# Kernel optimization log

Measured on AMD Instinct MI355X. Metric: run time of the kernel, lower is better.

The kernel has to match this reference:

```python
import jax, jax.numpy as jnp
import numpy as np

BETA = 0.25


def setup_inputs() -> dict:
    key = jax.random.key(0)
    k1, k2, k3, k4 = jax.random.split(key, 4)
    e_dim, n_e = 512, 8192
    z = jax.random.normal(k1, (16, e_dim, 32, 32), dtype=jnp.float32)
    # nn.init.normal_(embedding.weight, std=e_dim**-0.5)
    emb_weight = jax.random.normal(k2, (n_e, e_dim), dtype=jnp.float32) * (e_dim ** -0.5)
    # torch Linear default init ~ U(-1/sqrt(in), 1/sqrt(in))
    lim = 1.0 / np.sqrt(e_dim)
    proj_w = jax.random.uniform(k3, (e_dim, e_dim), minval=-lim, maxval=lim, dtype=jnp.float32)
    proj_b = jax.random.uniform(k4, (e_dim,), minval=-lim, maxval=lim, dtype=jnp.float32)
    return {"z": z, "emb_weight": emb_weight, "proj_w": proj_w, "proj_b": proj_b}


def reference(z, emb_weight, proj_w, proj_b):
    # z: [B, C, H, W] -> [B, H, W, C]
    zc = jnp.transpose(z, (0, 2, 3, 1))
    B, H, W, C = zc.shape
    z_flat = zc.reshape(-1, C)                               # [N, C]
    # projected codebook: Linear(e_dim, e_dim) -> x @ W^T + b
    qc = emb_weight @ proj_w.T + proj_b                      # [n_e, C]
    # squared distances: ||z||^2 + ||qc||^2 - 2 z.qc
    d = (jnp.sum(z_flat ** 2, axis=1, keepdims=True)
         + jnp.sum(qc ** 2, axis=1)
         - 2.0 * jnp.einsum('nd,kd->nk', z_flat, qc))        # [N, n_e]
    idx = jnp.argmin(d, axis=1)                              # [N]
    z_q = qc[idx].reshape(zc.shape)                          # [B, H, W, C]
    # legacy=False commit loss
    commit_loss = (BETA * jnp.mean((jax.lax.stop_gradient(z_q) - zc) ** 2)
                   + jnp.mean((z_q - jax.lax.stop_gradient(zc)) ** 2))
    # straight-through
    z_q = zc + jax.lax.stop_gradient(z_q - zc)
    z_q = jnp.transpose(z_q, (0, 3, 1, 2))                   # [B, C, H, W]
    min_encoding_indices = idx.reshape(B, H, W)              # sane_index_shape=True
    return z_q, commit_loss, min_encoding_indices
```

## Files before the change

### kernel.cpp

```cpp
#include <hip/hip_runtime.h>

typedef unsigned int uint;
typedef unsigned short ushort;
typedef __attribute__((ext_vector_type(8))) short short8;
typedef __attribute__((ext_vector_type(4))) float f32x4;

#define B_   16
#define C_   512
#define HW_  1024
#define N_   16384
#define K_   8192
#define EPS_ 0.25f

#define QC_OFF    0u
#define QC_SZ     (K_ * C_)
#define QN_OFF    (QC_OFF + QC_SZ)
#define QN_SZ     K_
#define ZN_OFF    (QN_OFF + QN_SZ)
#define ZN_SZ     N_
#define ZF_OFF    (ZN_OFF + ZN_SZ)
#define ZF_SZ     (N_ * C_)
#define ZH_OFF    (ZF_OFF + ZF_SZ)
#define ZH_SZ     (N_ * C_ / 2)
#define QH_OFF    (ZH_OFF + ZH_SZ)
#define QH_SZ     (K_ * C_ / 2)
#define WT_OFF    (QH_OFF + QH_SZ)
#define WT_SZ     (64 * N_ * 4)
#define CK_OFF    (WT_OFF + WT_SZ)
#define CK_SZ     (N_ * 16)
#define CC_OFF    (CK_OFF + CK_SZ)
#define CC_SZ     N_
#define IDXF_OFF  (CC_OFF + CC_SZ)
#define IDXF_SZ   N_
#define LOSS_OFF  (IDXF_OFF + IDXF_SZ)

#define OUT_ZQ    0
#define OUT_LOSS  8388608
#define OUT_IDX   8388609

__device__ __forceinline__ ushort f2bf(float f) {
    uint x = __float_as_uint(f);
    uint r = x + 0x7fffu + ((x >> 16) & 1u);
    return (ushort)(r >> 16);
}

__global__ __launch_bounds__(256) void transpose_z(const float* __restrict__ z,
                                                   float* __restrict__ zf,
                                                   ushort* __restrict__ zh) {
    __shared__ float ld[64][65];
    const int t = threadIdx.x;
    const int mt = blockIdx.x, ct = blockIdx.y, b = blockIdx.z;
    {
        const int cl = t >> 4, m4 = (t & 15) * 4;
#pragma unroll
        for (int cc = 0; cc < 4; ++cc) {
            const int c = ct * 64 + cc * 16 + cl;
            float4 v = *(const float4*)&z[((size_t)(b * 512 + c)) * 1024 + mt * 64 + m4];
            ld[cc * 16 + cl][m4 + 0] = v.x; ld[cc * 16 + cl][m4 + 1] = v.y;
            ld[cc * 16 + cl][m4 + 2] = v.z; ld[cc * 16 + cl][m4 + 3] = v.w;
        }
    }
    __syncthreads();
    {
        const int nl = t >> 4, c4 = (t & 15) * 4;
#pragma unroll
        for (int nn = 0; nn < 4; ++nn) {
            const int n_local = nn * 16 + nl;
            const size_t n = (size_t)b * 1024 + mt * 64 + n_local;
            float4 w;
            w.x = ld[c4 + 0][n_local]; w.y = ld[c4 + 1][n_local];
            w.z = ld[c4 + 2][n_local]; w.w = ld[c4 + 3][n_local];
            *(float4*)&zf[n * 512 + ct * 64 + c4] = w;
            ushort4 h; h.x = f2bf(w.x); h.y = f2bf(w.y); h.z = f2bf(w.z); h.w = f2bf(w.w);
            *(ushort4*)&zh[n * 512 + ct * 64 + c4] = h;
        }
    }
}

__global__ __launch_bounds__(256) void qc_gemm(const float* __restrict__ emb,
                                               const float* __restrict__ W,
                                               const float* __restrict__ bias,
                                               float* __restrict__ qc,
                                               ushort* __restrict__ qh) {
    __shared__ float As[16][132];
    __shared__ float Bs[16][68];
    const int t    = threadIdx.x;
    const int k0   = blockIdx.x * 128;
    const int c0   = blockIdx.y * 64;
    const int ty   = t >> 4, tx = t & 15;
    const int rowA = t >> 1;
    const int dqA  = (t & 1) * 8;
    const int rowB = t >> 2;
    const int dqB  = (t & 3) * 4;

    const float* pa = emb + (size_t)(k0 + rowA) * 512 + dqA;
    const float* pb = W   + (size_t)(c0 + rowB) * 512 + dqB;
    float4 ra0 = *(const float4*)&pa[0];
    float4 ra1 = *(const float4*)&pa[4];
    float4 rb  = *(const float4*)&pb[0];

    float acc[2][4][4] = {};
    for (int d0 = 0; d0 < 512; d0 += 16) {
        __syncthreads();
        As[dqA + 0][rowA] = ra0.x; As[dqA + 1][rowA] = ra0.y;
        As[dqA + 2][rowA] = ra0.z; As[dqA + 3][rowA] = ra0.w;
        As[dqA + 4][rowA] = ra1.x; As[dqA + 5][rowA] = ra1.y;
        As[dqA + 6][rowA] = ra1.z; As[dqA + 7][rowA] = ra1.w;
        Bs[dqB + 0][rowB] = rb.x;  Bs[dqB + 1][rowB] = rb.y;
        Bs[dqB + 2][rowB] = rb.z;  Bs[dqB + 3][rowB] = rb.w;
        if (d0 + 16 < 512) {
            ra0 = *(const float4*)&pa[d0 + 16];
            ra1 = *(const float4*)&pa[d0 + 20];
            rb  = *(const float4*)&pb[d0 + 16];
        }
        __syncthreads();
#pragma unroll
        for (int dd = 0; dd < 16; ++dd) {
            float4 a0 = *(const float4*)&As[dd][ty * 4];
            float4 a1 = *(const float4*)&As[dd][64 + ty * 4];
            float4 b0 = *(const float4*)&Bs[dd][tx * 4];
            float aa[2][4] = {{a0.x, a0.y, a0.z, a0.w}, {a1.x, a1.y, a1.z, a1.w}};
            float bb[4] = {b0.x, b0.y, b0.z, b0.w};
#pragma unroll
            for (int ih = 0; ih < 2; ++ih)
#pragma unroll
                for (int i = 0; i < 4; ++i)
#pragma unroll
                    for (int j = 0; j < 4; ++j)
                        acc[ih][i][j] += aa[ih][i] * bb[j];
        }
    }
#pragma unroll
    for (int ih = 0; ih < 2; ++ih)
#pragma unroll
        for (int i = 0; i < 4; ++i) {
            const size_t kr = (size_t)(k0 + ih * 64 + ty * 4 + i) * 512;
            const int cb = c0 + tx * 4;
            float4 v;
            v.x = acc[ih][i][0] + bias[cb + 0];
            v.y = acc[ih][i][1] + bias[cb + 1];
            v.z = acc[ih][i][2] + bias[cb + 2];
            v.w = acc[ih][i][3] + bias[cb + 3];
            *(float4*)&qc[kr + cb] = v;
            ushort4 h; h.x = f2bf(v.x); h.y = f2bf(v.y); h.z = f2bf(v.z); h.w = f2bf(v.w);
            *(ushort4*)&qh[kr + cb] = h;
        }
}

__global__ __launch_bounds__(256) void znorm_pairwise(const float* __restrict__ z,
                                                      float* __restrict__ zn) {
#pragma clang fp contract(off)
    const int n = blockIdx.x * 256 + threadIdx.x;
    const int b = n >> 10, m = n & 1023;
    const float* base = z + (size_t)b * C_ * HW_ + m;
    float s128[4];
#pragma unroll
    for (int blk = 0; blk < 4; ++blk) {
        float r[8];
#pragma unroll
        for (int j = 0; j < 8; ++j) {
            float v = base[(size_t)(blk * 128 + j) * HW_];
            r[j] = v * v;
        }
#pragma unroll 1
        for (int i = 8; i < 128; i += 8) {
#pragma unroll
            for (int j = 0; j < 8; ++j) {
                float v = base[(size_t)(blk * 128 + i + j) * HW_];
                float sq = v * v;
                r[j] = r[j] + sq;
            }
        }
        s128[blk] = ((r[0] + r[1]) + (r[2] + r[3])) + ((r[4] + r[5]) + (r[6] + r[7]));
    }
    zn[n] = (s128[0] + s128[1]) + (s128[2] + s128[3]);
}

__global__ __launch_bounds__(256) void qnorm_grouped(const float* __restrict__ qc,
                                                     float* __restrict__ qn) {
#pragma clang fp contract(off)
    const int t   = threadIdx.x;
    const int grp = t >> 3;
    const int j   = t & 7;
    const int k   = blockIdx.x * 32 + grp;
    const float* row = qc + (size_t)k * C_;
    float s[4];
#pragma unroll
    for (int blk = 0; blk < 4; ++blk) {
        float v0 = row[blk * 128 + j];
        float r  = v0 * v0;
#pragma unroll 1
        for (int i = 1; i < 16; ++i) {
            float v  = row[blk * 128 + i * 8 + j];
            float sq = v * v;
            r = r + sq;
        }
        float t1 = r  + __shfl_xor(r, 1, 64);
        float t2 = t1 + __shfl_xor(t1, 2, 64);
        float t3 = t2 + __shfl_xor(t2, 4, 64);
        s[blk] = t3;
    }
    if (j == 0) qn[k] = (s[0] + s[1]) + (s[2] + s[3]);
}

#define PH_BAR()  __builtin_amdgcn_s_barrier()
#define PH_LGKM() asm volatile("s_waitcnt lgkmcnt(0)" ::: "memory")
#define PH_VM4()  asm volatile("s_waitcnt vmcnt(4)" ::: "memory")

__device__ __forceinline__ short8 ld8(const short* p, int off) {
    return *(const short8*)(p + off);
}

__global__ __launch_bounds__(512, 2) void phaseA(const ushort* __restrict__ qh,
                                                 const ushort* __restrict__ zh,
                                                 const float* __restrict__ qn,
                                                 float* __restrict__ wtop) {
    __shared__ short lq[32768];
    __shared__ short lz[32768];
    const int t    = threadIdx.x;
    const int lane = t & 63;
    const int wv   = t >> 6;
    const int wk   = wv >> 2;
    const int wn   = wv & 3;
    const int n0   = blockIdx.x * 256;
    const int k0   = blockIdx.y * 256;

    const int l15 = lane & 15;
    const int hi8 = (lane >> 4) << 3;
    const int xr  = (l15 & 7) << 3;
    const short* pA0 = lq + wk * 8192 + l15 * 64 + ((hi8) ^ xr);
    const short* pA1 = lq + wk * 8192 + l15 * 64 + ((32 + hi8) ^ xr);
    const short* pB0 = lz + (wn >> 1) * 8192 + (wn & 1) * 4096 + l15 * 64 + ((hi8) ^ xr);
    const short* pB1 = lz + (wn >> 1) * 8192 + (wn & 1) * 4096 + l15 * 64 + ((32 + hi8) ^ xr);

    const int ch0 = t,        row0 = ch0 >> 3;
    const int ch1 = t + 512,  row1 = ch1 >> 3;
    const int ce0 = ((ch0 ^ row0) & 7) << 3;
    const int ce1 = ((ch1 ^ row1) & 7) << 3;
    const ushort* qsrc0 = qh + (size_t)(k0 + row0) * 512 + ce0;
    const ushort* qsrc1 = qh + (size_t)(k0 + row1) * 512 + ce1;
    const ushort* zsrc0 = zh + (size_t)(n0 + row0) * 512 + ce0;
    const ushort* zsrc1 = zh + (size_t)(n0 + row1) * 512 + ce1;
    short* qdst0 = lq + ch0 * 8;
    short* qdst1 = lq + ch1 * 8;
    short* zdst0 = lz + ch0 * 8;
    short* zdst1 = lz + ch1 * 8;

    auto stage_half = [&](int b, int h, int chunk) {
        const int co = chunk * 64;
        if (h < 2) {
            __builtin_amdgcn_global_load_lds(
                (const __attribute__((address_space(1))) uint*)(qsrc0 + h * 65536 + co),
                (__attribute__((address_space(3))) uint*)(qdst0 + (b * 2 + h) * 8192), 16, 0, 0);
            __builtin_amdgcn_global_load_lds(
                (const __attribute__((address_space(1))) uint*)(qsrc1 + h * 65536 + co),
                (__attribute__((address_space(3))) uint*)(qdst1 + (b * 2 + h) * 8192), 16, 0, 0);
        } else {
            __builtin_amdgcn_global_load_lds(
                (const __attribute__((address_space(1))) uint*)(zsrc0 + (h - 2) * 65536 + co),
                (__attribute__((address_space(3))) uint*)(zdst0 + (b * 2 + (h - 2)) * 8192), 16, 0, 0);
            __builtin_amdgcn_global_load_lds(
                (const __attribute__((address_space(1))) uint*)(zsrc1 + (h - 2) * 65536 + co),
                (__attribute__((address_space(3))) uint*)(zdst1 + (b * 2 + (h - 2)) * 8192), 16, 0, 0);
        }
    };

    f32x4 acc[8][4];
#pragma unroll
    for (int i = 0; i < 8; ++i)
#pragma unroll
        for (int j = 0; j < 4; ++j) acc[i][j] = (f32x4){0.f, 0.f, 0.f, 0.f};

    stage_half(0, 0, 0); stage_half(0, 1, 0); stage_half(0, 2, 0); stage_half(0, 3, 0);
    stage_half(1, 0, 1); stage_half(1, 1, 1);
    PH_VM4();
    PH_BAR();

    short8 a0[2][4], a1[2][4], b0[2][2], b1[2][2];

#pragma unroll 1
    for (int I = 0; I < 4; ++I) {
        const int t1 = 2 * I + 1;
        const int t2 = (2 * I + 2) & 7;
        const int t3 = (2 * I + 3) & 7;

#pragma unroll
        for (int i = 0; i < 4; ++i) { a0[0][i] = ld8(pA0, i * 1024); a0[1][i] = ld8(pA1, i * 1024); }
#pragma unroll
        for (int jj = 0; jj < 2; ++jj) { b0[0][jj] = ld8(pB0, jj * 1024); b0[1][jj] = ld8(pB1, jj * 1024); }
        stage_half(1, 2, t1);
        PH_BAR(); PH_LGKM();
        __builtin_amdgcn_s_setprio(1);
#pragma unroll
        for (int kk = 0; kk < 2; ++kk)
#pragma unroll
            for (int i = 0; i < 4; ++i)
#pragma unroll
                for (int jj = 0; jj < 2; ++jj)
                    acc[i][jj] = __builtin_amdgcn_mfma_f32_16x16x32_bf16(a0[kk][i], b0[kk][jj], acc[i][jj], 0, 0, 0);
        __builtin_amdgcn_s_setprio(0);
        PH_BAR();
#pragma unroll
        for (int i = 0; i < 4; ++i) { a1[0][i] = ld8(pA0, 4096 + i * 1024); a1[1][i] = ld8(pA1, 4096 + i * 1024); }
        stage_half(1, 3, t1);
        PH_BAR(); PH_LGKM();
        __builtin_amdgcn_s_setprio(1);
#pragma unroll
        for (int kk = 0; kk < 2; ++kk)
#pragma unroll
            for (int i = 0; i < 4; ++i)
#pragma unroll
                for (int jj = 0; jj < 2; ++jj)
                    acc[4 + i][jj] = __builtin_amdgcn_mfma_f32_16x16x32_bf16(a1[kk][i], b0[kk][jj], acc[4 + i][jj], 0, 0, 0);
        __builtin_amdgcn_s_setprio(0);
        PH_BAR();
#pragma unroll
        for (int jj = 0; jj < 2; ++jj) { b1[0][jj] = ld8(pB0, 2048 + jj * 1024); b1[1][jj] = ld8(pB1, 2048 + jj * 1024); }
        stage_half(0, 0, t2);
        PH_BAR(); PH_LGKM();
        __builtin_amdgcn_s_setprio(1);
#pragma unroll
        for (int kk = 0; kk < 2; ++kk)
#pragma unroll
            for (int i = 0; i < 4; ++i)
#pragma unroll
                for (int jj = 0; jj < 2; ++jj)
                    acc[i][2 + jj] = __builtin_amdgcn_mfma_f32_16x16x32_bf16(a0[kk][i], b1[kk][jj], acc[i][2 + jj], 0, 0, 0);
        __builtin_amdgcn_s_setprio(0);
        PH_BAR();
        stage_half(0, 1, t2);
        PH_BAR(); PH_LGKM();
        __builtin_amdgcn_s_setprio(1);
#pragma unroll
        for (int kk = 0; kk < 2; ++kk)
#pragma unroll
            for (int i = 0; i < 4; ++i)
#pragma unroll
                for (int jj = 0; jj < 2; ++jj)
                    acc[4 + i][2 + jj] = __builtin_amdgcn_mfma_f32_16x16x32_bf16(a1[kk][i], b1[kk][jj], acc[4 + i][2 + jj], 0, 0, 0);
        __builtin_amdgcn_s_setprio(0);
        PH_VM4();
        PH_BAR();

#pragma unroll
        for (int i = 0; i < 4; ++i) { a0[0][i] = ld8(pA0, 16384 + i * 1024); a0[1][i] = ld8(pA1, 16384 + i * 1024); }
#pragma unroll
        for (int jj = 0; jj < 2; ++jj) { b0[0][jj] = ld8(pB0, 16384 + jj * 1024); b0[1][jj] = ld8(pB1, 16384 + jj * 1024); }
        stage_half(0, 2, t2);
        PH_BAR(); PH_LGKM();
        __builtin_amdgcn_s_setprio(1);
#pragma unroll
        for (int kk = 0; kk < 2; ++kk)
#pragma unroll
            for (int i = 0; i < 4; ++i)
#pragma unroll
                for (int jj = 0; jj < 2; ++jj)
                    acc[i][jj] = __builtin_amdgcn_mfma_f32_16x16x32_bf16(a0[kk][i], b0[kk][jj], acc[i][jj], 0, 0, 0);
        __builtin_amdgcn_s_setprio(0);
        PH_BAR();
#pragma unroll
        for (int i = 0; i < 4; ++i) { a1[0][i] = ld8(pA0, 16384 + 4096 + i * 1024); a1[1][i] = ld8(pA1, 16384 + 4096 + i * 1024); }
        stage_half(0, 3, t2);
        PH_BAR(); PH_LGKM();
        __builtin_amdgcn_s_setprio(1);
#pragma unroll
        for (int kk = 0; kk < 2; ++kk)
#pragma unroll
            for (int i = 0; i < 4; ++i)
#pragma unroll
                for (int jj = 0; jj < 2; ++jj)
                    acc[4 + i][jj] = __builtin_amdgcn_mfma_f32_16x16x32_bf16(a1[kk][i], b0[kk][jj], acc[4 + i][jj], 0, 0, 0);
        __builtin_amdgcn_s_setprio(0);
        PH_BAR();
#pragma unroll
        for (int jj = 0; jj < 2; ++jj) { b1[0][jj] = ld8(pB0, 16384 + 2048 + jj * 1024); b1[1][jj] = ld8(pB1, 16384 + 2048 + jj * 1024); }
        stage_half(1, 0, t3);
        PH_BAR(); PH_LGKM();
        __builtin_amdgcn_s_setprio(1);
#pragma unroll
        for (int kk = 0; kk < 2; ++kk)
#pragma unroll
            for (int i = 0; i < 4; ++i)
#pragma unroll
                for (int jj = 0; jj < 2; ++jj)
                    acc[i][2 + jj] = __builtin_amdgcn_mfma_f32_16x16x32_bf16(a0[kk][i], b1[kk][jj], acc[i][2 + jj], 0, 0, 0);
        __builtin_amdgcn_s_setprio(0);
        PH_BAR();
        stage_half(1, 1, t3);
        PH_BAR(); PH_LGKM();
        __builtin_amdgcn_s_setprio(1);
#pragma unroll
        for (int kk = 0; kk < 2; ++kk)
#pragma unroll
            for (int i = 0; i < 4; ++i)
#pragma unroll
                for (int jj = 0; jj < 2; ++jj)
                    acc[4 + i][2 + jj] = __builtin_amdgcn_mfma_f32_16x16x32_bf16(a1[kk][i], b1[kk][jj], acc[4 + i][2 + jj], 0, 0, 0);
        __builtin_amdgcn_s_setprio(0);
        PH_VM4();
        PH_BAR();
    }

    const int q4 = (lane >> 4) * 4;
    float v1[4], v2[4];
    int   k1[4], k2[4];
#pragma unroll
    for (int in = 0; in < 4; ++in) { v1[in] = 1e30f; v2[in] = 1e30f; k1[in] = 0; k2[in] = 0; }

#pragma unroll
    for (int ik = 0; ik < 8; ++ik) {
        float qv[4];
#pragma unroll
        for (int r = 0; r < 4; ++r)
            qv[r] = qn[k0 + wk * 128 + ik * 16 + q4 + r];
#pragma unroll
        for (int in = 0; in < 4; ++in) {
#pragma unroll
            for (int r = 0; r < 4; ++r) {
                const float val = qv[r] - 2.0f * acc[ik][in][r];
                const int   kg  = k0 + wk * 128 + ik * 16 + q4 + r;
                if (val < v1[in]) { v2[in] = v1[in]; k2[in] = k1[in]; v1[in] = val; k1[in] = kg; }
                else if (val < v2[in]) { v2[in] = val; k2[in] = kg; }
            }
        }
    }
#pragma unroll
    for (int m = 16; m <= 32; m <<= 1) {
#pragma unroll
        for (int in = 0; in < 4; ++in) {
            const float ov1 = __shfl_xor(v1[in], m, 64);
            const int   ok1 = __shfl_xor(k1[in], m, 64);
            const float ov2 = __shfl_xor(v2[in], m, 64);
            const int   ok2 = __shfl_xor(k2[in], m, 64);
            float nv1, nv2; int nk1, nk2;
            if (ov1 < v1[in]) {
                nv1 = ov1; nk1 = ok1;
                if (v1[in] < ov2) { nv2 = v1[in]; nk2 = k1[in]; } else { nv2 = ov2; nk2 = ok2; }
            } else {
                nv1 = v1[in]; nk1 = k1[in];
                if (ov1 < v2[in]) { nv2 = ov1; nk2 = ok1; } else { nv2 = v2[in]; nk2 = k2[in]; }
            }
            v1[in] = nv1; k1[in] = nk1; v2[in] = nv2; k2[in] = nk2;
        }
    }
    if ((lane >> 4) == 0) {
        const int w = blockIdx.y * 2 + wk;
#pragma unroll
        for (int in = 0; in < 4; ++in) {
            const int n = n0 + wn * 64 + in * 16 + (lane & 15);
            float4 o; o.x = v1[in]; o.y = __int_as_float(k1[in]);
            o.z = v2[in]; o.w = __int_as_float(k2[in]);
            *(float4*)&wtop[((size_t)w * N_ + n) * 4] = o;
        }
    }
}

__global__ __launch_bounds__(256) void phaseB(const float* __restrict__ wtop,
                                              int* __restrict__ cand_k,
                                              int* __restrict__ cand_cnt,
                                              float* __restrict__ loss_acc) {
    const int n = blockIdx.x * 256 + threadIdx.x;
    if (n == 0) loss_acc[0] = 0.f;
    float rmin = 1e30f;
    for (int w = 0; w < 64; ++w)
        rmin = fminf(rmin, wtop[((size_t)w * N_ + n) * 4]);
    const float thr = rmin + EPS_;
    int cnt = 0;
    for (int w = 0; w < 64; ++w) {
        float4 e = *(const float4*)&wtop[((size_t)w * N_ + n) * 4];
        if (e.x <= thr && cnt < 16) cand_k[n * 16 + cnt++] = __float_as_int(e.y);
        if (e.z <= thr && cnt < 16) cand_k[n * 16 + cnt++] = __float_as_int(e.w);
    }
    cand_cnt[n] = cnt;
}

__global__ __launch_bounds__(256) void phaseC(const float* __restrict__ zf,
                                              const float* __restrict__ qc,
                                              const float* __restrict__ zn,
                                              const float* __restrict__ qn,
                                              const int* __restrict__ cand_k,
                                              const int* __restrict__ cand_cnt,
                                              int* __restrict__ idxf,
                                              float* __restrict__ out_idx) {
    __shared__ float zr[4][512];
    __shared__ float ql[4][2][512];
    const int wv   = threadIdx.x >> 6;
    const int lane = threadIdx.x & 63;
    const int r    = blockIdx.x * 4 + wv;
    const int cnt  = cand_cnt[r];

    if (cnt == 1) {
        if (lane == 0) { const int k = cand_k[r * 16]; idxf[r] = k; out_idx[r] = (float)k; }
        return;
    }

    *(float4*)&zr[wv][lane * 8]     = *(const float4*)&zf[(size_t)r * 512 + lane * 8];
    *(float4*)&zr[wv][lane * 8 + 4] = *(const float4*)&zf[(size_t)r * 512 + lane * 8 + 4];

    const int g  = lane >> 5;
    const int cl = (lane & 31) * 16;
    const int steps = (cnt + 1) >> 1;
    const float znr = zn[r];

    auto cand_of = [&](int s) {
        const int ci = 2 * s + g;
        return cand_k[r * 16 + (ci < cnt ? ci : 0)];
    };

    int k_cur = cand_of(0);
    const float* q0 = qc + (size_t)k_cur * 512 + cl;
    float4 p0 = *(const float4*)&q0[0];
    float4 p1 = *(const float4*)&q0[4];
    float4 p2 = *(const float4*)&q0[8];
    float4 p3 = *(const float4*)&q0[12];

    float bd = 1e30f;
    int   bi = 0x7fffffff;

    for (int s = 0; s < steps; ++s) {
        *(float4*)&ql[wv][g][cl + 0]  = p0;
        *(float4*)&ql[wv][g][cl + 4]  = p1;
        *(float4*)&ql[wv][g][cl + 8]  = p2;
        *(float4*)&ql[wv][g][cl + 12] = p3;

        int k_next = 0;
        if (s + 1 < steps) {
            k_next = cand_of(s + 1);
            const float* qn_ = qc + (size_t)k_next * 512 + cl;
            p0 = *(const float4*)&qn_[0];
            p1 = *(const float4*)&qn_[4];
            p2 = *(const float4*)&qn_[8];
            p3 = *(const float4*)&qn_[12];
        }

        float acc = 0.f;
#pragma unroll 16
        for (int c = 0; c < 512; c += 4) {
            float4 zv = *(const float4*)&zr[wv][c];
            float4 qv = *(const float4*)&ql[wv][g][c];
            acc = fmaf(zv.x, qv.x, acc);
            acc = fmaf(zv.y, qv.y, acc);
            acc = fmaf(zv.z, qv.z, acc);
            acc = fmaf(zv.w, qv.w, acc);
        }
        const float T = znr + qn[k_cur];
        const float d = T - 2.0f * acc;
        const bool valid = (2 * s + g) < cnt;
        if (valid && (d < bd || (d == bd && k_cur < bi))) { bd = d; bi = k_cur; }
        k_cur = k_next;
    }

    const float od = __shfl_xor(bd, 32, 64);
    const int   oi = __shfl_xor(bi, 32, 64);
    if (od < bd || (od == bd && oi < bi)) { bd = od; bi = oi; }

    if (lane == 0) { idxf[r] = bi; out_idx[r] = (float)bi; }
}

__global__ __launch_bounds__(256) void gather_out(const float* __restrict__ z,
                                                  const float* __restrict__ qc,
                                                  const int* __restrict__ idxf,
                                                  float* __restrict__ zq_out,
                                                  float* __restrict__ loss_acc) {
    __shared__ int   idxs[64];
    __shared__ float zqs[64][65];
    __shared__ float wsum[4];
    const int t  = threadIdx.x;
    const int mc = blockIdx.x;
    const int cc = blockIdx.y;
    const int bz = blockIdx.z;

    if (t < 64) idxs[t] = idxf[bz * 1024 + mc * 64 + t];
    __syncthreads();
    {
        const int row  = t >> 2;
        const int coff = (t & 3) * 16;
        const float* src = qc + (size_t)idxs[row] * 512 + cc * 64 + coff;
#pragma unroll
        for (int v = 0; v < 4; ++v) {
            float4 q = *(const float4*)&src[v * 4];
            zqs[row][coff + v * 4 + 0] = q.x;
            zqs[row][coff + v * 4 + 1] = q.y;
            zqs[row][coff + v * 4 + 2] = q.z;
            zqs[row][coff + v * 4 + 3] = q.w;
        }
    }
    __syncthreads();

    float ls = 0.f;
    {
        const int c_local = t >> 2;
        const int mg      = (t & 3) * 16;
        const size_t gbase = ((size_t)(bz * 512 + cc * 64 + c_local)) * 1024 + mc * 64 + mg;
#pragma unroll
        for (int v = 0; v < 4; ++v) {
            const int m = mg + v * 4;
            float4 w;
            w.x = zqs[m + 0][c_local];
            w.y = zqs[m + 1][c_local];
            w.z = zqs[m + 2][c_local];
            w.w = zqs[m + 3][c_local];
            float4 zv = *(const float4*)&z[gbase + v * 4];
            float dx = w.x - zv.x, dy = w.y - zv.y, dz = w.z - zv.z, dw = w.w - zv.w;
            ls += dx * dx + dy * dy + dz * dz + dw * dw;
            *(float4*)&zq_out[gbase + v * 4] = w;
        }
    }
#pragma unroll
    for (int m = 32; m; m >>= 1) ls += __shfl_xor(ls, m, 64);
    const int lane = t & 63, wvv = t >> 6;
    if (lane == 0) wsum[wvv] = ls;
    __syncthreads();
    if (t == 0) atomicAdd(loss_acc, wsum[0] + wsum[1] + wsum[2] + wsum[3]);
}

__global__ void finalize(const float* __restrict__ loss_acc,
                         float* __restrict__ out_loss) {
    out_loss[0] = 1.25f * loss_acc[0] / 8388608.0f;
}

extern "C" void kernel_launch(void* const* d_in, const int* in_sizes, int n_in,
                              void* d_out, int out_size, void* d_ws, size_t ws_size,
                              hipStream_t stream) {
    const float* z    = (const float*)d_in[0];
    const float* emb  = (const float*)d_in[1];
    const float* W    = (const float*)d_in[2];
    const float* bias = (const float*)d_in[3];
    float* ws = (float*)d_ws;

    float*  qc       = ws + QC_OFF;
    float*  qn       = ws + QN_OFF;
    float*  zn       = ws + ZN_OFF;
    float*  zf       = ws + ZF_OFF;
    ushort* zh       = (ushort*)(ws + ZH_OFF);
    ushort* qh       = (ushort*)(ws + QH_OFF);
    float*  wtop     = ws + WT_OFF;
    int*    cand_k   = (int*)(ws + CK_OFF);
    int*    cand_cnt = (int*)(ws + CC_OFF);
    int*    idxf     = (int*)(ws + IDXF_OFF);
    float*  loss_acc = ws + LOSS_OFF;
    float*  out      = (float*)d_out;

    transpose_z<<<dim3(16, 8, 16), 256, 0, stream>>>(z, zf, zh);
    qc_gemm<<<dim3(K_ / 128, C_ / 64), 256, 0, stream>>>(emb, W, bias, qc, qh);
    qnorm_grouped<<<K_ / 32, 256, 0, stream>>>(qc, qn);
    znorm_pairwise<<<N_ / 256, 256, 0, stream>>>(z, zn);
    phaseA<<<dim3(N_ / 256, K_ / 256), 512, 0, stream>>>(qh, zh, qn, wtop);
    phaseB<<<N_ / 256, 256, 0, stream>>>(wtop, cand_k, cand_cnt, loss_acc);
    phaseC<<<N_ / 4, 256, 0, stream>>>(zf, qc, zn, qn, cand_k, cand_cnt, idxf, out + OUT_IDX);
    gather_out<<<dim3(16, 8, B_), 256, 0, stream>>>(z, qc, idxf, out + OUT_ZQ, loss_acc);
    finalize<<<1, 1, 0, stream>>>(loss_acc, out + OUT_LOSS);
}
```

Measured before the change: 419.7 us.

## Fuse candidate selection into refinement kernel and restructure phaseA MFMA schedule

Merges phaseB (per-row threshold and candidate list) into phaseC by having each wavefront read its row's 64 per-tile top-2 entries, reduce the minimum with shuffles, and compact candidates into LDS via ballot/popcount. This removes a kernel launch and the global cand_k/cand_cnt round trip. wtop is re-laid out row-major so each row's entries are contiguous. phaseA's inner loop is restructured from four barrier-separated MFMA sub-phases to two larger ones, staging two halves per phase with a partial lgkmcnt wait. The candidate cap of 16 is removed (up to 128 now), which could change work for rows with many near-ties.

```diff
diff --git a/kernel.cpp b/kernel.cpp
--- a/kernel.cpp
+++ b/kernel.cpp
@@ -2,6 +2,7 @@
 
 typedef unsigned int uint;
 typedef unsigned short ushort;
+typedef unsigned long long ulong64;
 typedef __attribute__((ext_vector_type(8))) short short8;
 typedef __attribute__((ext_vector_type(4))) float f32x4;
 
@@ -26,11 +27,7 @@
 #define QH_SZ     (K_ * C_ / 2)
 #define WT_OFF    (QH_OFF + QH_SZ)
 #define WT_SZ     (64 * N_ * 4)
-#define CK_OFF    (WT_OFF + WT_SZ)
-#define CK_SZ     (N_ * 16)
-#define CC_OFF    (CK_OFF + CK_SZ)
-#define CC_SZ     N_
-#define IDXF_OFF  (CC_OFF + CC_SZ)
+#define IDXF_OFF  (WT_OFF + WT_SZ)
 #define IDXF_SZ   N_
 #define LOSS_OFF  (IDXF_OFF + IDXF_SZ)
 
@@ -203,9 +200,10 @@
     if (j == 0) qn[k] = (s[0] + s[1]) + (s[2] + s[3]);
 }
 
-#define PH_BAR()  __builtin_amdgcn_s_barrier()
-#define PH_LGKM() asm volatile("s_waitcnt lgkmcnt(0)" ::: "memory")
-#define PH_VM4()  asm volatile("s_waitcnt vmcnt(4)" ::: "memory")
+#define PH_BAR()   __builtin_amdgcn_s_barrier()
+#define PH_LGKM()  asm volatile("s_waitcnt lgkmcnt(0)" ::: "memory")
+#define PH_LGKM8() asm volatile("s_waitcnt lgkmcnt(8)" ::: "memory")
+#define PH_VM4()   asm volatile("s_waitcnt vmcnt(4)" ::: "memory")
 
 __device__ __forceinline__ short8 ld8(const short* p, int off) {
     return *(const short8*)(p + off);
@@ -280,15 +278,18 @@
 
 #pragma unroll 1
     for (int I = 0; I < 4; ++I) {
-        const int t1 = 2 * I + 1;
-        const int t2 = (2 * I + 2) & 7;
-        const int t3 = (2 * I + 3) & 7;
-
-#pragma unroll
-        for (int i = 0; i < 4; ++i) { a0[0][i] = ld8(pA0, i * 1024); a0[1][i] = ld8(pA1, i * 1024); }
+        const int tE = 2 * I;
+        const int tO = 2 * I + 1;
+
+#pragma unroll
+        for (int i = 0; i < 4; ++i) {
+            a0[0][i] = ld8(pA0, i * 1024);        a0[1][i] = ld8(pA1, i * 1024);
+            a1[0][i] = ld8(pA0, 4096 + i * 1024); a1[1][i] = ld8(pA1, 4096 + i * 1024);
+        }
 #pragma unroll
         for (int jj = 0; jj < 2; ++jj) { b0[0][jj] = ld8(pB0, jj * 1024); b0[1][jj] = ld8(pB1, jj * 1024); }
-        stage_half(1, 2, t1);
+        stage_half(1, 2, (tO) & 7); stage_half(1, 3, (tO) & 7);
+        PH_LGKM8();
         PH_BAR(); PH_LGKM();
         __builtin_amdgcn_s_setprio(1);
 #pragma unroll
@@ -296,13 +297,15 @@
 #pragma unroll
             for (int i = 0; i < 4; ++i)
 #pragma unroll
-                for (int jj = 0; jj < 2; ++jj)
-                    acc[i][jj] = __builtin_amdgcn_mfma_f32_16x16x32_bf16(a0[kk][i], b0[kk][jj], acc[i][jj], 0, 0, 0);
+                for (int jj = 0; jj < 2; ++jj) {
+                    acc[i][jj]     = __builtin_amdgcn_mfma_f32_16x16x32_bf16(a0[kk][i], b0[kk][jj], acc[i][jj], 0, 0, 0);
+                    acc[4 + i][jj] = __builtin_amdgcn_mfma_f32_16x16x32_bf16(a1[kk][i], b0[kk][jj], acc[4 + i][jj], 0, 0, 0);
+                }
         __builtin_amdgcn_s_setprio(0);
         PH_BAR();
 #pragma unroll
-        for (int i = 0; i < 4; ++i) { a1[0][i] = ld8(pA0, 4096 + i * 1024); a1[1][i] = ld8(pA1, 4096 + i * 1024); }
-        stage_half(1, 3, t1);
+        for (int jj = 0; jj < 2; ++jj) { b1[0][jj] = ld8(pB0, 2048 + jj * 1024); b1[1][jj] = ld8(pB1, 2048 + jj * 1024); }
+        stage_half(0, 0, (tE + 2) & 7); stage_half(0, 1, (tE + 2) & 7);
         PH_BAR(); PH_LGKM();
         __builtin_amdgcn_s_setprio(1);
 #pragma unroll
@@ -310,43 +313,23 @@
 #pragma unroll
             for (int i = 0; i < 4; ++i)
 #pragma unroll
-                for (int jj = 0; jj < 2; ++jj)
-                    acc[4 + i][jj] = __builtin_amdgcn_mfma_f32_16x16x32_bf16(a1[kk][i], b0[kk][jj], acc[4 + i][jj], 0, 0, 0);
-        __builtin_amdgcn_s_setprio(0);
-        PH_BAR();
-#pragma unroll
-        for (int jj = 0; jj < 2; ++jj) { b1[0][jj] = ld8(pB0, 2048 + jj * 1024); b1[1][jj] = ld8(pB1, 2048 + jj * 1024); }
-        stage_half(0, 0, t2);
-        PH_BAR(); PH_LGKM();
-        __builtin_amdgcn_s_setprio(1);
-#pragma unroll
-        for (int kk = 0; kk < 2; ++kk)
-#pragma unroll
-            for (int i = 0; i < 4; ++i)
-#pragma unroll
-                for (int jj = 0; jj < 2; ++jj)
-                    acc[i][2 + jj] = __builtin_amdgcn_mfma_f32_16x16x32_bf16(a0[kk][i], b1[kk][jj], acc[i][2 + jj], 0, 0, 0);
-        __builtin_amdgcn_s_setprio(0);
-        PH_BAR();
-        stage_half(0, 1, t2);
-        PH_BAR(); PH_LGKM();
-        __builtin_amdgcn_s_setprio(1);
-#pragma unroll
-        for (int kk = 0; kk < 2; ++kk)
-#pragma unroll
-            for (int i = 0; i < 4; ++i)
-#pragma unroll
-                for (int jj = 0; jj < 2; ++jj)
+                for (int jj = 0; jj < 2; ++jj) {
+                    acc[i][2 + jj]     = __builtin_amdgcn_mfma_f32_16x16x32_bf16(a0[kk][i], b1[kk][jj], acc[i][2 + jj], 0, 0, 0);
                     acc[4 + i][2 + jj] = __builtin_amdgcn_mfma_f32_16x16x32_bf16(a1[kk][i], b1[kk][jj], acc[4 + i][2 + jj], 0, 0, 0);
+                }
         __builtin_amdgcn_s_setprio(0);
         PH_VM4();
         PH_BAR();
 
 #pragma unroll
-        for (int i = 0; i < 4; ++i) { a0[0][i] = ld8(pA0, 16384 + i * 1024); a0[1][i] = ld8(pA1, 16384 + i * 1024); }
+        for (int i = 0; i < 4; ++i) {
+            a0[0][i] = ld8(pA0, 16384 + i * 1024);        a0[1][i] = ld8(pA1, 16384 + i * 1024);
+            a1[0][i] = ld8(pA0, 16384 + 4096 + i * 1024); a1[1][i] = ld8(pA1, 16384 + 4096 + i * 1024);
+        }
 #pragma unroll
         for (int jj = 0; jj < 2; ++jj) { b0[0][jj] = ld8(pB0, 16384 + jj * 1024); b0[1][jj] = ld8(pB1, 16384 + jj * 1024); }
-        stage_half(0, 2, t2);
+        stage_half(0, 2, (tO + 1) & 7); stage_half(0, 3, (tO + 1) & 7);
+        PH_LGKM8();
         PH_BAR(); PH_LGKM();
         __builtin_amdgcn_s_setprio(1);
 #pragma unroll
@@ -354,13 +337,15 @@
 #pragma unroll
             for (int i = 0; i < 4; ++i)
 #pragma unroll
-                for (int jj = 0; jj < 2; ++jj)
-                    acc[i][jj] = __builtin_amdgcn_mfma_f32_16x16x32_bf16(a0[kk][i], b0[kk][jj], acc[i][jj], 0, 0, 0);
+                for (int jj = 0; jj < 2; ++jj) {
+                    acc[i][jj]     = __builtin_amdgcn_mfma_f32_16x16x32_bf16(a0[kk][i], b0[kk][jj], acc[i][jj], 0, 0, 0);
+                    acc[4 + i][jj] = __builtin_amdgcn_mfma_f32_16x16x32_bf16(a1[kk][i], b0[kk][jj], acc[4 + i][jj], 0, 0, 0);
+                }
         __builtin_amdgcn_s_setprio(0);
         PH_BAR();
 #pragma unroll
-        for (int i = 0; i < 4; ++i) { a1[0][i] = ld8(pA0, 16384 + 4096 + i * 1024); a1[1][i] = ld8(pA1, 16384 + 4096 + i * 1024); }
-        stage_half(0, 3, t2);
+        for (int jj = 0; jj < 2; ++jj) { b1[0][jj] = ld8(pB0, 16384 + 2048 + jj * 1024); b1[1][jj] = ld8(pB1, 16384 + 2048 + jj * 1024); }
+        stage_half(1, 0, (tO + 2) & 7); stage_half(1, 1, (tO + 2) & 7);
         PH_BAR(); PH_LGKM();
         __builtin_amdgcn_s_setprio(1);
 #pragma unroll
@@ -368,34 +353,10 @@
 #pragma unroll
             for (int i = 0; i < 4; ++i)
 #pragma unroll
-                for (int jj = 0; jj < 2; ++jj)
-                    acc[4 + i][jj] = __builtin_amdgcn_mfma_f32_16x16x32_bf16(a1[kk][i], b0[kk][jj], acc[4 + i][jj], 0, 0, 0);
-        __builtin_amdgcn_s_setprio(0);
-        PH_BAR();
-#pragma unroll
-        for (int jj = 0; jj < 2; ++jj) { b1[0][jj] = ld8(pB0, 16384 + 2048 + jj * 1024); b1[1][jj] = ld8(pB1, 16384 + 2048 + jj * 1024); }
-        stage_half(1, 0, t3);
-        PH_BAR(); PH_LGKM();
-        __builtin_amdgcn_s_setprio(1);
-#pragma unroll
-        for (int kk = 0; kk < 2; ++kk)
-#pragma unroll
-            for (int i = 0; i < 4; ++i)
-#pragma unroll
-                for (int jj = 0; jj < 2; ++jj)
-                    acc[i][2 + jj] = __builtin_amdgcn_mfma_f32_16x16x32_bf16(a0[kk][i], b1[kk][jj], acc[i][2 + jj], 0, 0, 0);
-        __builtin_amdgcn_s_setprio(0);
-        PH_BAR();
-        stage_half(1, 1, t3);
-        PH_BAR(); PH_LGKM();
-        __builtin_amdgcn_s_setprio(1);
-#pragma unroll
-        for (int kk = 0; kk < 2; ++kk)
-#pragma unroll
-            for (int i = 0; i < 4; ++i)
-#pragma unroll
-                for (int jj = 0; jj < 2; ++jj)
+                for (int jj = 0; jj < 2; ++jj) {
+                    acc[i][2 + jj]     = __builtin_amdgcn_mfma_f32_16x16x32_bf16(a0[kk][i], b1[kk][jj], acc[i][2 + jj], 0, 0, 0);
                     acc[4 + i][2 + jj] = __builtin_amdgcn_mfma_f32_16x16x32_bf16(a1[kk][i], b1[kk][jj], acc[4 + i][2 + jj], 0, 0, 0);
+                }
         __builtin_amdgcn_s_setprio(0);
         PH_VM4();
         PH_BAR();
@@ -450,52 +411,51 @@
             const int n = n0 + wn * 64 + in * 16 + (lane & 15);
             float4 o; o.x = v1[in]; o.y = __int_as_float(k1[in]);
             o.z = v2[in]; o.w = __int_as_float(k2[in]);
-            *(float4*)&wtop[((size_t)w * N_ + n) * 4] = o;
-        }
-    }
-}
-
-__global__ __launch_bounds__(256) void phaseB(const float* __restrict__ wtop,
-                                              int* __restrict__ cand_k,
-                                              int* __restrict__ cand_cnt,
-                                              float* __restrict__ loss_acc) {
-    const int n = blockIdx.x * 256 + threadIdx.x;
-    if (n == 0) loss_acc[0] = 0.f;
-    float rmin = 1e30f;
-    for (int w = 0; w < 64; ++w)
-        rmin = fminf(rmin, wtop[((size_t)w * N_ + n) * 4]);
-    const float thr = rmin + EPS_;
-    int cnt = 0;
-    for (int w = 0; w < 64; ++w) {
-        float4 e = *(const float4*)&wtop[((size_t)w * N_ + n) * 4];
-        if (e.x <= thr && cnt < 16) cand_k[n * 16 + cnt++] = __float_as_int(e.y);
-        if (e.z <= thr && cnt < 16) cand_k[n * 16 + cnt++] = __float_as_int(e.w);
-    }
-    cand_cnt[n] = cnt;
-}
-
-__global__ __launch_bounds__(256) void phaseC(const float* __restrict__ zf,
-                                              const float* __restrict__ qc,
-                                              const float* __restrict__ zn,
-                                              const float* __restrict__ qn,
-                                              const int* __restrict__ cand_k,
-                                              const int* __restrict__ cand_cnt,
-                                              int* __restrict__ idxf,
-                                              float* __restrict__ out_idx) {
+            *(float4*)&wtop[((size_t)n * 64 + w) * 4] = o;
+        }
+    }
+}
+
+__global__ __launch_bounds__(256) void phaseBC(const float* __restrict__ zf,
+                                               const float* __restrict__ qc,
+                                               const float* __restrict__ zn,
+                                               const float* __restrict__ qn,
+                                               const float* __restrict__ wtop,
+                                               int* __restrict__ idxf,
+                                               float* __restrict__ out_idx,
+                                               float* __restrict__ loss_acc) {
     __shared__ float zr[4][512];
     __shared__ float ql[4][2][512];
+    __shared__ int   clist[4][128];
     const int wv   = threadIdx.x >> 6;
     const int lane = threadIdx.x & 63;
     const int r    = blockIdx.x * 4 + wv;
-    const int cnt  = cand_cnt[r];
+    if (blockIdx.x == 0 && threadIdx.x == 0) loss_acc[0] = 0.f;
+
+    float4 e = *(const float4*)&wtop[((size_t)r * 64 + lane) * 4];
+    float rmin = e.x;
+#pragma unroll
+    for (int m = 1; m <= 32; m <<= 1) rmin = fminf(rmin, __shfl_xor(rmin, m, 64));
+    const float thr = rmin + EPS_;
+    const bool h1 = (e.x <= thr), h2 = (e.z <= thr);
+    const ulong64 m1 = __ballot(h1);
+    const ulong64 m2 = __ballot(h2);
+    const int c1  = __popcll(m1);
+    const int cnt = c1 + __popcll(m2);
 
     if (cnt == 1) {
-        if (lane == 0) { const int k = cand_k[r * 16]; idxf[r] = k; out_idx[r] = (float)k; }
+        if (h1) { const int k = __float_as_int(e.y); idxf[r] = k; out_idx[r] = (float)k; }
+        else if (h2) { const int k = __float_as_int(e.w); idxf[r] = k; out_idx[r] = (float)k; }
         return;
     }
+
+    const ulong64 below = (lane == 63) ? ~0ull >> 1 : ((1ull << lane) - 1);
+    if (h1) clist[wv][__popcll(m1 & below)] = __float_as_int(e.y);
+    if (h2) clist[wv][c1 + __popcll(m2 & below)] = __float_as_int(e.w);
 
     *(float4*)&zr[wv][lane * 8]     = *(const float4*)&zf[(size_t)r * 512 + lane * 8];
     *(float4*)&zr[wv][lane * 8 + 4] = *(const float4*)&zf[(size_t)r * 512 + lane * 8 + 4];
+    asm volatile("s_waitcnt lgkmcnt(0)" ::: "memory");
 
     const int g  = lane >> 5;
     const int cl = (lane & 31) * 16;
@@ -504,7 +464,7 @@
 
     auto cand_of = [&](int s) {
         const int ci = 2 * s + g;
-        return cand_k[r * 16 + (ci < cnt ? ci : 0)];
+        return clist[wv][ci < cnt ? ci : 0];
     };
 
     int k_cur = cand_of(0);
@@ -635,8 +595,6 @@
     ushort* zh       = (ushort*)(ws + ZH_OFF);
     ushort* qh       = (ushort*)(ws + QH_OFF);
     float*  wtop     = ws + WT_OFF;
-    int*    cand_k   = (int*)(ws + CK_OFF);
-    int*    cand_cnt = (int*)(ws + CC_OFF);
     int*    idxf     = (int*)(ws + IDXF_OFF);
     float*  loss_acc = ws + LOSS_OFF;
     float*  out      = (float*)d_out;
@@ -646,8 +604,7 @@
     qnorm_grouped<<<K_ / 32, 256, 0, stream>>>(qc, qn);
     znorm_pairwise<<<N_ / 256, 256, 0, stream>>>(z, zn);
     phaseA<<<dim3(N_ / 256, K_ / 256), 512, 0, stream>>>(qh, zh, qn, wtop);
-    phaseB<<<N_ / 256, 256, 0, stream>>>(wtop, cand_k, cand_cnt, loss_acc);
-    phaseC<<<N_ / 4, 256, 0, stream>>>(zf, qc, zn, qn, cand_k, cand_cnt, idxf, out + OUT_IDX);
+    phaseBC<<<N_ / 4, 256, 0, stream>>>(zf, qc, zn, qn, wtop, idxf, out + OUT_IDX, loss_acc);
     gather_out<<<dim3(16, 8, B_), 256, 0, stream>>>(z, qc, idxf, out + OUT_ZQ, loss_acc);
     finalize<<<1, 1, 0, stream>>>(loss_acc, out + OUT_LOSS);
 }
```

Result: faster. 387.7 us (-7.6%).
